# Performance work log

Measured on AMD Instinct MI355X. Metric: run time of the kernel, lower is better.

## Reference

```python
import jax, jax.numpy as jnp
import numpy as np
import math

BATCH, CLS, ATT_DIM, IMG_DIM = 256, 500, 1024, 1024
ATT_HC, HIDDEN_C = 256, 1024
T_TEMP = 10.0
DEGREE = 30
THRESH = math.cos(math.pi * DEGREE / 180.0)
NEG = -9.0e15


def setup_inputs() -> dict:
    key = jax.random.key(0)
    ks = jax.random.split(key, 9)
    inp = {
        "image_feats": jax.random.normal(ks[0], (BATCH, IMG_DIM), dtype=jnp.float32),
        "attributes": jax.random.normal(ks[1], (CLS, ATT_DIM), dtype=jnp.float32),
        "unused": 0,
        # learned parameters (kaiming-like scaling)
        "att_g": jax.random.normal(ks[2], (ATT_DIM, ATT_HC), dtype=jnp.float32) / math.sqrt(ATT_DIM),
        "img_w": jax.random.normal(ks[3], (IMG_DIM, HIDDEN_C), dtype=jnp.float32) / math.sqrt(IMG_DIM),
        "sem_w": jax.random.normal(ks[4], (ATT_DIM, HIDDEN_C), dtype=jnp.float32) / math.sqrt(ATT_DIM),
        "sem_b": jax.random.normal(ks[5], (1, HIDDEN_C), dtype=jnp.float32) / math.sqrt(IMG_DIM),
        "fc_w": jax.random.normal(ks[6], (1, HIDDEN_C), dtype=jnp.float32) / math.sqrt(HIDDEN_C),
        "fc_b": jax.random.normal(ks[7], (1,), dtype=jnp.float32) / math.sqrt(HIDDEN_C),
    }
    return inp


def _get_new_attribute(attributes, att_g):
    # project attributes, cosine similarity between all class pairs
    g = attributes @ att_g                                    # [cls, att_hC]
    gn = g / jnp.linalg.norm(g, axis=1, keepdims=True)        # row-normalize
    sim = gn @ gn.T                                           # [cls, cls] cosine sims
    raw = jnp.where(sim > THRESH, sim, NEG)                   # angular-threshold mask
    attention = jax.nn.softmax(raw * T_TEMP, axis=1)          # [cls, cls]
    return attention @ attributes                             # [cls, att_dim]


def reference(image_feats, attributes, unused, att_g, img_w, sem_w, sem_b, fc_w, fc_b):
    att_outs = _get_new_attribute(attributes, att_g)          # [cls, att_dim]
    # factor the broadcast: identical math to matmul on expanded tensors
    img_h = image_feats @ img_w                               # [batch, hidden]
    sem_h = att_outs @ sem_w                                  # [cls, hidden]
    hidden = jax.nn.relu(img_h[:, None, :] + sem_h[None, :, :] + sem_b[None, :, :])  # [batch, cls, hidden]
    out = jnp.einsum('bch,h->bc', hidden, fc_w[0]) + fc_b[0]  # [batch, cls]
    return out
```

## Files before the change

### kernel.cpp

```cpp
#include <hip/hip_runtime.h>
#include <math.h>

#define BATCH 256
#define CLS 500
#define T_TEMP_ 10.0f
#define THRESH_ 0.86602540378443864676f
#define NEGV -9.0e15f

typedef __attribute__((ext_vector_type(8))) short short8;
typedef __attribute__((ext_vector_type(8))) unsigned short u16x8;
typedef __attribute__((ext_vector_type(4))) unsigned short u16x4;
typedef __attribute__((ext_vector_type(4))) float f32x4;
typedef __attribute__((ext_vector_type(2))) float f32x2;

static __device__ __forceinline__ unsigned short f2bf(float x) {
    unsigned int u = __builtin_bit_cast(unsigned int, x);
    u += 0x7fff + ((u >> 16) & 1);
    return (unsigned short)(u >> 16);
}
static __device__ __forceinline__ float bf2f(unsigned short v) {
    return __builtin_bit_cast(float, (unsigned int)v << 16);
}
static __device__ __forceinline__ float fel(const float4& v, int j) { return (&v.x)[j]; }
static __device__ __forceinline__ u16x8 pack8(const float4& a, const float4& b) {
    u16x8 o;
    o[0] = f2bf(a.x); o[1] = f2bf(a.y); o[2] = f2bf(a.z); o[3] = f2bf(a.w);
    o[4] = f2bf(b.x); o[5] = f2bf(b.y); o[6] = f2bf(b.z); o[7] = f2bf(b.w);
    return o;
}

__global__ __launch_bounds__(256) void gpart_kernel(
    const float* __restrict__ attrs, const float* __restrict__ attg,
    float* __restrict__ gpart)
{
    __shared__ unsigned short As[64][40];
    __shared__ unsigned short Bs[128][40];
    const int t = threadIdx.x;
    const int bid = blockIdx.x;
    const int mt = bid >> 4, nt = (bid >> 3) & 1, split = bid & 7;
    const int n0 = nt * 128, ar0 = mt * 64, k0 = split * 128;

    const int w = t >> 6, lane = t & 63;
    const int wr = w >> 1, wc = w & 1;
    const int fr = lane & 15, kg = lane >> 4;
    const int as_row = t >> 2, as_kq = t & 3;
    const int bs_nc = (t & 31) * 4, bs_kr = t >> 5;

    f32x4 acc[2][4];
    #pragma unroll
    for (int i = 0; i < 2; ++i)
        #pragma unroll
        for (int j = 0; j < 4; ++j) acc[i][j] = (f32x4){0.f, 0.f, 0.f, 0.f};

    for (int kb = k0; kb < k0 + 128; kb += 32) {
        {
            const int gr = ar0 + as_row;
            float4 v0 = make_float4(0.f,0.f,0.f,0.f), v1 = v0;
            if (gr < CLS) {
                const float* ap = &attrs[(size_t)gr * 1024 + kb + as_kq * 8];
                v0 = *(const float4*)ap; v1 = *(const float4*)(ap + 4);
            }
            *(u16x8*)&As[as_row][as_kq * 8] = pack8(v0, v1);
        }
        {
            const float* bp = &attg[(size_t)(kb + bs_kr * 4) * 256 + n0 + bs_nc];
            float4 r0 = *(const float4*)(bp);
            float4 r1 = *(const float4*)(bp + 256);
            float4 r2 = *(const float4*)(bp + 512);
            float4 r3 = *(const float4*)(bp + 768);
            #pragma unroll
            for (int j = 0; j < 4; ++j) {
                unsigned int lo = (unsigned int)f2bf(fel(r0, j)) | ((unsigned int)f2bf(fel(r1, j)) << 16);
                unsigned int hi = (unsigned int)f2bf(fel(r2, j)) | ((unsigned int)f2bf(fel(r3, j)) << 16);
                uint2 u2; u2.x = lo; u2.y = hi;
                *(uint2*)&Bs[bs_nc + j][bs_kr * 4] = u2;
            }
        }
        __syncthreads();
        short8 af[2], bfr[4];
        #pragma unroll
        for (int i = 0; i < 2; ++i) af[i] = *(short8*)&As[wr * 32 + i * 16 + fr][kg * 8];
        #pragma unroll
        for (int j = 0; j < 4; ++j) bfr[j] = *(short8*)&Bs[wc * 64 + j * 16 + fr][kg * 8];
        #pragma unroll
        for (int i = 0; i < 2; ++i)
            #pragma unroll
            for (int j = 0; j < 4; ++j)
                acc[i][j] = __builtin_amdgcn_mfma_f32_16x16x32_bf16(af[i], bfr[j], acc[i][j], 0, 0, 0);
        __syncthreads();
    }

    float* Gp = gpart + (size_t)split * (512 * 256);
    const int orow0 = ar0 + wr * 32, ocol0 = n0 + wc * 64;
    #pragma unroll
    for (int i = 0; i < 2; ++i) {
        const int r0 = orow0 + i * 16 + kg * 4;
        #pragma unroll
        for (int j = 0; j < 4; ++j) {
            const int cc = ocol0 + j * 16 + fr;
            #pragma unroll
            for (int r = 0; r < 4; ++r)
                Gp[(size_t)(r0 + r) * 256 + cc] = acc[i][j][r];
        }
    }
}

__global__ __launch_bounds__(256) void reduce_norm_kernel(
    const float* __restrict__ part, unsigned short* __restrict__ gn_bf)
{
    const int c = blockIdx.x, t = threadIdx.x;
    float v = 0.f;
    #pragma unroll
    for (int z = 0; z < 8; ++z) v += part[(size_t)z * (512 * 256) + c * 256 + t];
    float ss = v * v;
    #pragma unroll
    for (int off = 32; off >= 1; off >>= 1) ss += __shfl_down(ss, off);
    __shared__ float red[4];
    const int wave = t >> 6, lane = t & 63;
    if (lane == 0) red[wave] = ss;
    __syncthreads();
    const float tot = red[0] + red[1] + red[2] + red[3];
    const float rn  = 1.f / sqrtf(tot);
    gn_bf[c * 256 + t] = f2bf(v * rn);
}

__global__ __launch_bounds__(256) void mfma_gemm_bf(
    const unsigned short* __restrict__ A1, int alim1,
    const unsigned short* __restrict__ A2, int a2t0, int alim2,
    const unsigned short* __restrict__ B1, const unsigned short* __restrict__ B2,
    float* __restrict__ C, unsigned short* __restrict__ Cbf,
    int M, int N, int K, int klen)
{
    __shared__ unsigned short As[64][40];
    __shared__ unsigned short Bs[128][40];

    const int t  = threadIdx.x;
    const int bx = blockIdx.x;
    const int n0 = blockIdx.y * 128;
    const int k0 = blockIdx.z * klen;

    const unsigned short* A; const unsigned short* B; int ar0, alim;
    if (bx < a2t0) { A = A1; B = B1; ar0 = bx * 64;          alim = alim1; }
    else           { A = A2; B = B2; ar0 = (bx - a2t0) * 64; alim = alim2; }

    const int w = t >> 6, lane = t & 63;
    const int wr = w >> 1, wc = w & 1;
    const int fr = lane & 15, kg = lane >> 4;

    const int a_row = t >> 2, a_k = (t & 3) * 8;
    const int b_row = t >> 1, b_k = (t & 1) * 16;
    const int gra = ar0 + a_row;
    const int grb = n0 + b_row;
    const bool va = gra < alim;
    const bool vb = grb < N;
    const size_t abase = (size_t)gra * K + a_k;
    const size_t bbase = (size_t)grb * K + b_k;

    u16x8 zz = {0,0,0,0,0,0,0,0};
    u16x8 pa = zz, pb0 = zz, pb1 = zz;
    if (va) pa = *(const u16x8*)&A[abase + k0];
    if (vb) { pb0 = *(const u16x8*)&B[bbase + k0]; pb1 = *(const u16x8*)&B[bbase + k0 + 8]; }

    f32x4 acc[2][4];
    #pragma unroll
    for (int i = 0; i < 2; ++i)
        #pragma unroll
        for (int j = 0; j < 4; ++j) acc[i][j] = (f32x4){0.f, 0.f, 0.f, 0.f};

    for (int kb = k0; kb < k0 + klen; kb += 32) {
        *(u16x8*)&As[a_row][a_k] = pa;
        *(u16x8*)&Bs[b_row][b_k] = pb0;
        *(u16x8*)&Bs[b_row][b_k + 8] = pb1;
        __syncthreads();

        const int kn = kb + 32;
        if (kn < k0 + klen) {
            if (va) pa = *(const u16x8*)&A[abase + kn];
            if (vb) { pb0 = *(const u16x8*)&B[bbase + kn]; pb1 = *(const u16x8*)&B[bbase + kn + 8]; }
        }

        short8 af[2], bfr[4];
        #pragma unroll
        for (int i = 0; i < 2; ++i) af[i] = *(short8*)&As[wr * 32 + i * 16 + fr][kg * 8];
        #pragma unroll
        for (int j = 0; j < 4; ++j) bfr[j] = *(short8*)&Bs[wc * 64 + j * 16 + fr][kg * 8];
        #pragma unroll
        for (int i = 0; i < 2; ++i)
            #pragma unroll
            for (int j = 0; j < 4; ++j)
                acc[i][j] = __builtin_amdgcn_mfma_f32_16x16x32_bf16(af[i], bfr[j], acc[i][j], 0, 0, 0);
        __syncthreads();
    }

    const int orow0 = bx * 64 + wr * 32, ocol0 = n0 + wc * 64;
    if (Cbf) {
        unsigned short* Cw = Cbf + (size_t)blockIdx.z * M * N;
        #pragma unroll
        for (int i = 0; i < 2; ++i) {
            const int r0 = orow0 + i * 16 + kg * 4;
            #pragma unroll
            for (int j = 0; j < 4; ++j) {
                const int cc = ocol0 + j * 16 + fr;
                if (cc >= N) continue;
                #pragma unroll
                for (int r = 0; r < 4; ++r) {
                    const int rr = r0 + r;
                    if (rr < M) Cw[(size_t)rr * N + cc] = f2bf(acc[i][j][r]);
                }
            }
        }
    } else {
        float* Cw = C + (gridDim.z > 1 ? (size_t)blockIdx.z * M * N : 0);
        #pragma unroll
        for (int i = 0; i < 2; ++i) {
            const int r0 = orow0 + i * 16 + kg * 4;
            #pragma unroll
            for (int j = 0; j < 4; ++j) {
                const int cc = ocol0 + j * 16 + fr;
                if (cc >= N) continue;
                #pragma unroll
                for (int r = 0; r < 4; ++r) {
                    const int rr = r0 + r;
                    if (rr < M) Cw[(size_t)rr * N + cc] = acc[i][j][r];
                }
            }
        }
    }
}

__global__ __launch_bounds__(256) void softmax_att_kernel(
    const float* __restrict__ sim, const float* __restrict__ attrs,
    unsigned short* __restrict__ att_outs)
{
    const int c = blockIdx.x, t = threadIdx.x;
    __shared__ float p_s[512];
    __shared__ float redm[4];
    __shared__ float reds[4];

    const float d0 = sim[(size_t)c * CLS + t];
    const float d1 = (t + 256 < CLS) ? sim[(size_t)c * CLS + t + 256] : NEGV;

    float vmax = fmaxf((d0 > THRESH_) ? d0 : NEGV, (d1 > THRESH_) ? d1 : NEGV);
    #pragma unroll
    for (int off = 32; off >= 1; off >>= 1) vmax = fmaxf(vmax, __shfl_down(vmax, off));
    const int wave = t >> 6, lane = t & 63;
    if (lane == 0) redm[wave] = vmax;
    __syncthreads();
    const float m = fmaxf(fmaxf(redm[0], redm[1]), fmaxf(redm[2], redm[3]));

    const float p0 = (d0 > THRESH_) ? expf(T_TEMP_ * (d0 - m)) : 0.f;
    const float p1 = (d1 > THRESH_) ? expf(T_TEMP_ * (d1 - m)) : 0.f;
    p_s[t] = p0;
    p_s[t + 256] = p1;
    float vsum = p0 + p1;
    #pragma unroll
    for (int off = 32; off >= 1; off >>= 1) vsum += __shfl_down(vsum, off);
    if (lane == 0) reds[wave] = vsum;
    __syncthreads();
    const float inv = 1.f / (reds[0] + reds[1] + reds[2] + reds[3]);

    float acc[4] = {0.f, 0.f, 0.f, 0.f};
    for (int base = 0; base < 512; base += 64) {
        const float pv_l = p_s[base + lane];
        unsigned long long mask = __ballot(pv_l > 0.f);
        while (mask) {
            const int l = __ffsll((long long)mask) - 1;
            mask &= mask - 1;
            const int c2 = base + l;
            const float pv = p_s[c2];
            const float* ar = &attrs[(size_t)c2 * 1024 + t];
            #pragma unroll
            for (int j = 0; j < 4; ++j) acc[j] += pv * ar[256 * j];
        }
    }
    #pragma unroll
    for (int j = 0; j < 4; ++j)
        att_outs[(size_t)c * 1024 + t + 256 * j] = f2bf(acc[j] * inv);
}

__global__ __launch_bounds__(256) void hid_kernel(
    const float* __restrict__ imgf, const unsigned short* __restrict__ atto_bf,
    const float* __restrict__ imgw, const float* __restrict__ semw,
    unsigned short* __restrict__ hidP)
{
    __shared__ unsigned short As[64][40];
    __shared__ unsigned short Bs[128][40];
    const int t = threadIdx.x;
    const int mt = blockIdx.x, nt = blockIdx.y, split = blockIdx.z;
    const int n0 = nt * 128, k0 = split * 256;
    const bool img_side = (mt < 4);
    const int ar0 = img_side ? mt * 64 : (mt - 4) * 64;
    const int alim = img_side ? 256 : 500;
    const float* Bf = img_side ? imgw : semw;

    const int w = t >> 6, lane = t & 63;
    const int wr = w >> 1, wc = w & 1;
    const int fr = lane & 15, kg = lane >> 4;
    const int as_row = t >> 2, as_kq = t & 3;
    const int bs_nc = (t & 31) * 4, bs_kr = t >> 5;

    f32x4 acc[2][4];
    #pragma unroll
    for (int i = 0; i < 2; ++i)
        #pragma unroll
        for (int j = 0; j < 4; ++j) acc[i][j] = (f32x4){0.f, 0.f, 0.f, 0.f};

    for (int kb = k0; kb < k0 + 256; kb += 32) {
        {
            const int gr = ar0 + as_row;
            if (img_side) {
                float4 v0 = make_float4(0.f,0.f,0.f,0.f), v1 = v0;
                if (gr < alim) {
                    const float* ap = &imgf[(size_t)gr * 1024 + kb + as_kq * 8];
                    v0 = *(const float4*)ap; v1 = *(const float4*)(ap + 4);
                }
                *(u16x8*)&As[as_row][as_kq * 8] = pack8(v0, v1);
            } else {
                u16x8 pa = {0,0,0,0,0,0,0,0};
                if (gr < alim) pa = *(const u16x8*)&atto_bf[(size_t)gr * 1024 + kb + as_kq * 8];
                *(u16x8*)&As[as_row][as_kq * 8] = pa;
            }
        }
        {
            const float* bp = &Bf[(size_t)(kb + bs_kr * 4) * 1024 + n0 + bs_nc];
            float4 r0 = *(const float4*)(bp);
            float4 r1 = *(const float4*)(bp + 1024);
            float4 r2 = *(const float4*)(bp + 2048);
            float4 r3 = *(const float4*)(bp + 3072);
            #pragma unroll
            for (int j = 0; j < 4; ++j) {
                unsigned int lo = (unsigned int)f2bf(fel(r0, j)) | ((unsigned int)f2bf(fel(r1, j)) << 16);
                unsigned int hi = (unsigned int)f2bf(fel(r2, j)) | ((unsigned int)f2bf(fel(r3, j)) << 16);
                uint2 u2; u2.x = lo; u2.y = hi;
                *(uint2*)&Bs[bs_nc + j][bs_kr * 4] = u2;
            }
        }
        __syncthreads();
        short8 af[2], bfr[4];
        #pragma unroll
        for (int i = 0; i < 2; ++i) af[i] = *(short8*)&As[wr * 32 + i * 16 + fr][kg * 8];
        #pragma unroll
        for (int j = 0; j < 4; ++j) bfr[j] = *(short8*)&Bs[wc * 64 + j * 16 + fr][kg * 8];
        #pragma unroll
        for (int i = 0; i < 2; ++i)
            #pragma unroll
            for (int j = 0; j < 4; ++j)
                acc[i][j] = __builtin_amdgcn_mfma_f32_16x16x32_bf16(af[i], bfr[j], acc[i][j], 0, 0, 0);
        __syncthreads();
    }

    unsigned short* Cw = hidP + (size_t)split * (756 * 1024);
    const int orow0 = mt * 64 + wr * 32, ocol0 = n0 + wc * 64;
    #pragma unroll
    for (int i = 0; i < 2; ++i) {
        const int r0 = orow0 + i * 16 + kg * 4;
        #pragma unroll
        for (int j = 0; j < 4; ++j) {
            const int cc = ocol0 + j * 16 + fr;
            #pragma unroll
            for (int r = 0; r < 4; ++r) {
                const int rr = r0 + r;
                if (rr < 756) Cw[(size_t)rr * 1024 + cc] = f2bf(acc[i][j][r]);
            }
        }
    }
}

__global__ __launch_bounds__(256) void fused_out_partial(
    const unsigned short* __restrict__ part, const float* __restrict__ sem_b,
    const float* __restrict__ fc_w, float* __restrict__ outpart)
{
    __shared__ float imgs[64][36];
    __shared__ float sems[64][36];
    __shared__ float fcs[32];

    const size_t pstride = (size_t)756 * 1024;
    const int t  = threadIdx.x;
    const int tb = t >> 4, tc = t & 15;
    const int b0 = blockIdx.x * 64, c0 = blockIdx.y * 64;
    const int h0 = blockIdx.z * 32;

    if (t < 8) *(float4*)&fcs[t * 4] = *(const float4*)&fc_w[h0 + t * 4];

    {
        const int row = t >> 2, col = (t & 3) * 8;
        f32x4 iv0 = {0.f,0.f,0.f,0.f}, iv1 = iv0;
        const unsigned short* pi = &part[(size_t)(b0 + row) * 1024 + h0 + col];
        #pragma unroll
        for (int z = 0; z < 4; ++z) {
            u16x8 vz = *(const u16x8*)(pi + (size_t)z * pstride);
            iv0[0] += bf2f(vz[0]); iv0[1] += bf2f(vz[1]);
            iv0[2] += bf2f(vz[2]); iv0[3] += bf2f(vz[3]);
            iv1[0] += bf2f(vz[4]); iv1[1] += bf2f(vz[5]);
            iv1[2] += bf2f(vz[6]); iv1[3] += bf2f(vz[7]);
        }
        *(f32x4*)&imgs[row][col]     = iv0;
        *(f32x4*)&imgs[row][col + 4] = iv1;

        f32x4 sv0 = {0.f,0.f,0.f,0.f}, sv1 = sv0;
        if (c0 + row < CLS) {
            const unsigned short* ps2 = &part[(size_t)(256 + c0 + row) * 1024 + h0 + col];
            #pragma unroll
            for (int z = 0; z < 4; ++z) {
                u16x8 vz = *(const u16x8*)(ps2 + (size_t)z * pstride);
                sv0[0] += bf2f(vz[0]); sv0[1] += bf2f(vz[1]);
                sv0[2] += bf2f(vz[2]); sv0[3] += bf2f(vz[3]);
                sv1[0] += bf2f(vz[4]); sv1[1] += bf2f(vz[5]);
                sv1[2] += bf2f(vz[6]); sv1[3] += bf2f(vz[7]);
            }
            sv0 += *(const f32x4*)&sem_b[h0 + col];
            sv1 += *(const f32x4*)&sem_b[h0 + col + 4];
        }
        *(f32x4*)&sems[row][col]     = sv0;
        *(f32x4*)&sems[row][col + 4] = sv1;
    }
    __syncthreads();

    f32x2 acc2[4][4];
    #pragma unroll
    for (int i = 0; i < 4; ++i)
        #pragma unroll
        for (int j = 0; j < 4; ++j) acc2[i][j] = (f32x2){0.f, 0.f};

    #pragma unroll
    for (int h4 = 0; h4 < 8; ++h4) {
        f32x4 ia[4], sa[4];
        #pragma unroll
        for (int i = 0; i < 4; ++i) ia[i] = *(f32x4*)&imgs[tb + 16 * i][h4 * 4];
        #pragma unroll
        for (int j = 0; j < 4; ++j) sa[j] = *(f32x4*)&sems[tc + 16 * j][h4 * 4];
        const f32x4 wv = *(const f32x4*)&fcs[h4 * 4];
        #pragma unroll
        for (int e2 = 0; e2 < 2; ++e2) {
            const f32x2 w2 = {wv[2 * e2], wv[2 * e2 + 1]};
            f32x2 ia2[4], sa2[4];
            #pragma unroll
            for (int i = 0; i < 4; ++i) ia2[i] = (f32x2){ia[i][2 * e2], ia[i][2 * e2 + 1]};
            #pragma unroll
            for (int j = 0; j < 4; ++j) sa2[j] = (f32x2){sa[j][2 * e2], sa[j][2 * e2 + 1]};
            #pragma unroll
            for (int i = 0; i < 4; ++i)
                #pragma unroll
                for (int j = 0; j < 4; ++j) {
                    f32x2 s = ia2[i] + sa2[j];
                    s = __builtin_elementwise_max(s, (f32x2){0.f, 0.f});
                    acc2[i][j] += s * w2;
                }
        }
    }

    const int nh = blockIdx.z;
    #pragma unroll
    for (int i = 0; i < 4; ++i) {
        const int b = b0 + tb + 16 * i;
        #pragma unroll
        for (int j = 0; j < 4; ++j) {
            const int cc = c0 + tc + 16 * j;
            if (cc < CLS)
                outpart[((size_t)nh * BATCH + b) * CLS + cc] = acc2[i][j][0] + acc2[i][j][1];
        }
    }
}

__global__ __launch_bounds__(256) void finalize_kernel(
    const float* __restrict__ partial, const float* __restrict__ fc_b,
    float* __restrict__ out)
{
    const int idx = blockIdx.x * 256 + threadIdx.x;
    if (idx >= BATCH * CLS) return;
    float s = fc_b[0];
    #pragma unroll
    for (int nh = 0; nh < 32; ++nh)
        s += partial[(size_t)nh * (BATCH * CLS) + idx];
    out[idx] = s;
}

extern "C" void kernel_launch(void* const* d_in, const int* in_sizes, int n_in,
                              void* d_out, int out_size, void* d_ws, size_t ws_size,
                              hipStream_t stream)
{
    const float* imgf  = (const float*)d_in[0];
    const float* attrs = (const float*)d_in[1];
    const float* attg  = (const float*)d_in[3];
    const float* imgw  = (const float*)d_in[4];
    const float* semw  = (const float*)d_in[5];
    const float* semb  = (const float*)d_in[6];
    const float* fcw   = (const float*)d_in[7];
    const float* fcb   = (const float*)d_in[8];
    float* out = (float*)d_out;

    char* ws = (char*)d_ws;
    size_t off = 0;
    auto alloc = [&](size_t b) { size_t o = off; off = (off + b + 255) & ~(size_t)255; return o; };
    float* gpart          = (float*)(ws + alloc((size_t)8 * 512 * 256 * 4));
    unsigned short* gn_bf = (unsigned short*)(ws + alloc((size_t)500 * 256 * 2));
    float* sim            = (float*)(ws + alloc((size_t)CLS * CLS * 4));
    unsigned short* atto  = (unsigned short*)(ws + alloc((size_t)500 * 1024 * 2));
    unsigned short* hidP  = (unsigned short*)(ws + alloc((size_t)4 * 756 * 1024 * 2));
    float* outP           = (float*)(ws + alloc((size_t)32 * BATCH * CLS * 4));

    gpart_kernel<<<128, 256, 0, stream>>>(attrs, attg, gpart);
    reduce_norm_kernel<<<CLS, 256, 0, stream>>>(gpart, gn_bf);
    mfma_gemm_bf<<<dim3(8, 4, 1), 256, 0, stream>>>(
        gn_bf, 500, gn_bf, 1000, 500, gn_bf, gn_bf,
        sim, nullptr, 500, 500, 256, 256);
    softmax_att_kernel<<<CLS, 256, 0, stream>>>(sim, attrs, atto);
    hid_kernel<<<dim3(12, 8, 4), 256, 0, stream>>>(imgf, atto, imgw, semw, hidP);
    fused_out_partial<<<dim3(4, 8, 32), 256, 0, stream>>>(hidP, semb, fcw, outP);
    finalize_kernel<<<(BATCH * CLS + 255) / 256, 256, 0, stream>>>(outP, fcb, out);
}
```

Baseline: 67.01 us.

## Reassociate attention matmul to gather projected attributes and fuse GEMMs into one launch

```diff
diff --git a/kernel.cpp b/kernel.cpp
--- a/kernel.cpp
+++ b/kernel.cpp
@@ -29,16 +29,17 @@
     return o;
 }
 
-__global__ __launch_bounds__(256) void gpart_kernel(
+__global__ __launch_bounds__(256) void mega_gemm(
     const float* __restrict__ attrs, const float* __restrict__ attg,
-    float* __restrict__ gpart)
+    const float* __restrict__ imgf, const float* __restrict__ imgw,
+    const float* __restrict__ semw,
+    float* __restrict__ gpart, unsigned short* __restrict__ imgP,
+    unsigned short* __restrict__ asemP)
 {
     __shared__ unsigned short As[64][40];
     __shared__ unsigned short Bs[128][40];
     const int t = threadIdx.x;
     const int bid = blockIdx.x;
-    const int mt = bid >> 4, nt = (bid >> 3) & 1, split = bid & 7;
-    const int n0 = nt * 128, ar0 = mt * 64, k0 = split * 128;
 
     const int w = t >> 6, lane = t & 63;
     const int wr = w >> 1, wc = w & 1;
@@ -46,28 +47,49 @@
     const int as_row = t >> 2, as_kq = t & 3;
     const int bs_nc = (t & 31) * 4, bs_kr = t >> 5;
 
+    const float* A; const float* Bf;
+    int ar0, alim, n0, k0, klen, bstride, split;
+    if (bid < 128) {
+        const int mt = bid >> 4, nt = (bid >> 3) & 1; split = bid & 7;
+        A = attrs; alim = CLS; ar0 = mt * 64;
+        Bf = attg; bstride = 256; n0 = nt * 128;
+        k0 = split * 128; klen = 128;
+    } else if (bid < 192) {
+        const int idx = bid - 128; split = idx & 1;
+        const int nt = (idx >> 1) & 7, mt = idx >> 4;
+        A = imgf; alim = 256; ar0 = mt * 64;
+        Bf = imgw; bstride = 1024; n0 = nt * 128;
+        k0 = split * 512; klen = 512;
+    } else {
+        const int idx = bid - 192; split = idx & 1;
+        const int nt = (idx >> 1) & 7, mt = idx >> 4;
+        A = attrs; alim = CLS; ar0 = mt * 64;
+        Bf = semw; bstride = 1024; n0 = nt * 128;
+        k0 = split * 512; klen = 512;
+    }
+
     f32x4 acc[2][4];
     #pragma unroll
     for (int i = 0; i < 2; ++i)
         #pragma unroll
         for (int j = 0; j < 4; ++j) acc[i][j] = (f32x4){0.f, 0.f, 0.f, 0.f};
 
-    for (int kb = k0; kb < k0 + 128; kb += 32) {
+    for (int kb = k0; kb < k0 + klen; kb += 32) {
         {
             const int gr = ar0 + as_row;
             float4 v0 = make_float4(0.f,0.f,0.f,0.f), v1 = v0;
-            if (gr < CLS) {
-                const float* ap = &attrs[(size_t)gr * 1024 + kb + as_kq * 8];
+            if (gr < alim) {
+                const float* ap = &A[(size_t)gr * 1024 + kb + as_kq * 8];
                 v0 = *(const float4*)ap; v1 = *(const float4*)(ap + 4);
             }
             *(u16x8*)&As[as_row][as_kq * 8] = pack8(v0, v1);
         }
         {
-            const float* bp = &attg[(size_t)(kb + bs_kr * 4) * 256 + n0 + bs_nc];
+            const float* bp = &Bf[(size_t)(kb + bs_kr * 4) * bstride + n0 + bs_nc];
             float4 r0 = *(const float4*)(bp);
-            float4 r1 = *(const float4*)(bp + 256);
-            float4 r2 = *(const float4*)(bp + 512);
-            float4 r3 = *(const float4*)(bp + 768);
+            float4 r1 = *(const float4*)(bp + bstride);
+            float4 r2 = *(const float4*)(bp + 2 * bstride);
+            float4 r3 = *(const float4*)(bp + 3 * bstride);
             #pragma unroll
             for (int j = 0; j < 4; ++j) {
                 unsigned int lo = (unsigned int)f2bf(fel(r0, j)) | ((unsigned int)f2bf(fel(r1, j)) << 16);
@@ -90,17 +112,34 @@
         __syncthreads();
     }
 
-    float* Gp = gpart + (size_t)split * (512 * 256);
     const int orow0 = ar0 + wr * 32, ocol0 = n0 + wc * 64;
-    #pragma unroll
-    for (int i = 0; i < 2; ++i) {
-        const int r0 = orow0 + i * 16 + kg * 4;
-        #pragma unroll
-        for (int j = 0; j < 4; ++j) {
-            const int cc = ocol0 + j * 16 + fr;
-            #pragma unroll
-            for (int r = 0; r < 4; ++r)
-                Gp[(size_t)(r0 + r) * 256 + cc] = acc[i][j][r];
+    if (bid < 128) {
+        float* Gp = gpart + (size_t)split * (512 * 256);
+        #pragma unroll
+        for (int i = 0; i < 2; ++i) {
+            const int r0 = orow0 + i * 16 + kg * 4;
+            #pragma unroll
+            for (int j = 0; j < 4; ++j) {
+                const int cc = ocol0 + j * 16 + fr;
+                #pragma unroll
+                for (int r = 0; r < 4; ++r)
+                    Gp[(size_t)(r0 + r) * 256 + cc] = acc[i][j][r];
+            }
+        }
+    } else {
+        unsigned short* Cw = (bid < 192)
+            ? imgP  + (size_t)split * (256 * 1024)
+            : asemP + (size_t)split * (512 * 1024);
+        #pragma unroll
+        for (int i = 0; i < 2; ++i) {
+            const int r0 = orow0 + i * 16 + kg * 4;
+            #pragma unroll
+            for (int j = 0; j < 4; ++j) {
+                const int cc = ocol0 + j * 16 + fr;
+                #pragma unroll
+                for (int r = 0; r < 4; ++r)
+                    Cw[(size_t)(r0 + r) * 1024 + cc] = f2bf(acc[i][j][r]);
+            }
         }
     }
 }
@@ -124,42 +163,31 @@
     gn_bf[c * 256 + t] = f2bf(v * rn);
 }
 
-__global__ __launch_bounds__(256) void mfma_gemm_bf(
-    const unsigned short* __restrict__ A1, int alim1,
-    const unsigned short* __restrict__ A2, int a2t0, int alim2,
-    const unsigned short* __restrict__ B1, const unsigned short* __restrict__ B2,
-    float* __restrict__ C, unsigned short* __restrict__ Cbf,
-    int M, int N, int K, int klen)
+__global__ __launch_bounds__(256) void sim_kernel(
+    const unsigned short* __restrict__ gn, float* __restrict__ S)
 {
     __shared__ unsigned short As[64][40];
     __shared__ unsigned short Bs[128][40];
-
     const int t  = threadIdx.x;
-    const int bx = blockIdx.x;
-    const int n0 = blockIdx.y * 128;
-    const int k0 = blockIdx.z * klen;
-
-    const unsigned short* A; const unsigned short* B; int ar0, alim;
-    if (bx < a2t0) { A = A1; B = B1; ar0 = bx * 64;          alim = alim1; }
-    else           { A = A2; B = B2; ar0 = (bx - a2t0) * 64; alim = alim2; }
+    const int ar0 = blockIdx.x * 64;
+    const int n0  = blockIdx.y * 128;
 
     const int w = t >> 6, lane = t & 63;
     const int wr = w >> 1, wc = w & 1;
     const int fr = lane & 15, kg = lane >> 4;
-
     const int a_row = t >> 2, a_k = (t & 3) * 8;
     const int b_row = t >> 1, b_k = (t & 1) * 16;
     const int gra = ar0 + a_row;
     const int grb = n0 + b_row;
-    const bool va = gra < alim;
-    const bool vb = grb < N;
-    const size_t abase = (size_t)gra * K + a_k;
-    const size_t bbase = (size_t)grb * K + b_k;
+    const bool va = gra < CLS;
+    const bool vb = grb < CLS;
+    const size_t abase = (size_t)gra * 256 + a_k;
+    const size_t bbase = (size_t)grb * 256 + b_k;
 
     u16x8 zz = {0,0,0,0,0,0,0,0};
     u16x8 pa = zz, pb0 = zz, pb1 = zz;
-    if (va) pa = *(const u16x8*)&A[abase + k0];
-    if (vb) { pb0 = *(const u16x8*)&B[bbase + k0]; pb1 = *(const u16x8*)&B[bbase + k0 + 8]; }
+    if (va) pa = *(const u16x8*)&gn[abase];
+    if (vb) { pb0 = *(const u16x8*)&gn[bbase]; pb1 = *(const u16x8*)&gn[bbase + 8]; }
 
     f32x4 acc[2][4];
     #pragma unroll
@@ -167,16 +195,16 @@
         #pragma unroll
         for (int j = 0; j < 4; ++j) acc[i][j] = (f32x4){0.f, 0.f, 0.f, 0.f};
 
-    for (int kb = k0; kb < k0 + klen; kb += 32) {
+    for (int kb = 0; kb < 256; kb += 32) {
         *(u16x8*)&As[a_row][a_k] = pa;
         *(u16x8*)&Bs[b_row][b_k] = pb0;
         *(u16x8*)&Bs[b_row][b_k + 8] = pb1;
         __syncthreads();
 
         const int kn = kb + 32;
-        if (kn < k0 + klen) {
-            if (va) pa = *(const u16x8*)&A[abase + kn];
-            if (vb) { pb0 = *(const u16x8*)&B[bbase + kn]; pb1 = *(const u16x8*)&B[bbase + kn + 8]; }
+        if (kn < 256) {
+            if (va) pa = *(const u16x8*)&gn[abase + kn];
+            if (vb) { pb0 = *(const u16x8*)&gn[bbase + kn]; pb1 = *(const u16x8*)&gn[bbase + kn + 8]; }
         }
 
         short8 af[2], bfr[4];
@@ -192,45 +220,26 @@
         __syncthreads();
     }
 
-    const int orow0 = bx * 64 + wr * 32, ocol0 = n0 + wc * 64;
-    if (Cbf) {
-        unsigned short* Cw = Cbf + (size_t)blockIdx.z * M * N;
-        #pragma unroll
-        for (int i = 0; i < 2; ++i) {
-            const int r0 = orow0 + i * 16 + kg * 4;
-            #pragma unroll
-            for (int j = 0; j < 4; ++j) {
-                const int cc = ocol0 + j * 16 + fr;
-                if (cc >= N) continue;
-                #pragma unroll
-                for (int r = 0; r < 4; ++r) {
-                    const int rr = r0 + r;
-                    if (rr < M) Cw[(size_t)rr * N + cc] = f2bf(acc[i][j][r]);
-                }
+    const int orow0 = ar0 + wr * 32, ocol0 = n0 + wc * 64;
+    #pragma unroll
+    for (int i = 0; i < 2; ++i) {
+        const int r0 = orow0 + i * 16 + kg * 4;
+        #pragma unroll
+        for (int j = 0; j < 4; ++j) {
+            const int cc = ocol0 + j * 16 + fr;
+            if (cc >= CLS) continue;
+            #pragma unroll
+            for (int r = 0; r < 4; ++r) {
+                const int rr = r0 + r;
+                if (rr < CLS) S[(size_t)rr * CLS + cc] = acc[i][j][r];
             }
         }
-    } else {
-        float* Cw = C + (gridDim.z > 1 ? (size_t)blockIdx.z * M * N : 0);
-        #pragma unroll
-        for (int i = 0; i < 2; ++i) {
-            const int r0 = orow0 + i * 16 + kg * 4;
-            #pragma unroll
-            for (int j = 0; j < 4; ++j) {
-                const int cc = ocol0 + j * 16 + fr;
-                if (cc >= N) continue;
-                #pragma unroll
-                for (int r = 0; r < 4; ++r) {
-                    const int rr = r0 + r;
-                    if (rr < M) Cw[(size_t)rr * N + cc] = acc[i][j][r];
-                }
-            }
-        }
-    }
-}
-
-__global__ __launch_bounds__(256) void softmax_att_kernel(
-    const float* __restrict__ sim, const float* __restrict__ attrs,
-    unsigned short* __restrict__ att_outs)
+    }
+}
+
+__global__ __launch_bounds__(256) void softmax_gather_kernel(
+    const float* __restrict__ sim, const unsigned short* __restrict__ asemP,
+    const float* __restrict__ semb, unsigned short* __restrict__ sem_h)
 {
     const int c = blockIdx.x, t = threadIdx.x;
     __shared__ float p_s[512];
@@ -268,113 +277,28 @@
             mask &= mask - 1;
             const int c2 = base + l;
             const float pv = p_s[c2];
-            const float* ar = &attrs[(size_t)c2 * 1024 + t];
-            #pragma unroll
-            for (int j = 0; j < 4; ++j) acc[j] += pv * ar[256 * j];
+            const unsigned short* a0 = &asemP[(size_t)c2 * 1024 + t];
+            const unsigned short* a1 = a0 + (size_t)512 * 1024;
+            #pragma unroll
+            for (int j = 0; j < 4; ++j)
+                acc[j] += pv * (bf2f(a0[256 * j]) + bf2f(a1[256 * j]));
         }
     }
     #pragma unroll
     for (int j = 0; j < 4; ++j)
-        att_outs[(size_t)c * 1024 + t + 256 * j] = f2bf(acc[j] * inv);
-}
-
-__global__ __launch_bounds__(256) void hid_kernel(
-    const float* __restrict__ imgf, const unsigned short* __restrict__ atto_bf,
-    const float* __restrict__ imgw, const float* __restrict__ semw,
-    unsigned short* __restrict__ hidP)
-{
-    __shared__ unsigned short As[64][40];
-    __shared__ unsigned short Bs[128][40];
-    const int t = threadIdx.x;
-    const int mt = blockIdx.x, nt = blockIdx.y, split = blockIdx.z;
-    const int n0 = nt * 128, k0 = split * 256;
-    const bool img_side = (mt < 4);
-    const int ar0 = img_side ? mt * 64 : (mt - 4) * 64;
-    const int alim = img_side ? 256 : 500;
-    const float* Bf = img_side ? imgw : semw;
-
-    const int w = t >> 6, lane = t & 63;
-    const int wr = w >> 1, wc = w & 1;
-    const int fr = lane & 15, kg = lane >> 4;
-    const int as_row = t >> 2, as_kq = t & 3;
-    const int bs_nc = (t & 31) * 4, bs_kr = t >> 5;
-
-    f32x4 acc[2][4];
-    #pragma unroll
-    for (int i = 0; i < 2; ++i)
-        #pragma unroll
-        for (int j = 0; j < 4; ++j) acc[i][j] = (f32x4){0.f, 0.f, 0.f, 0.f};
-
-    for (int kb = k0; kb < k0 + 256; kb += 32) {
-        {
-            const int gr = ar0 + as_row;
-            if (img_side) {
-                float4 v0 = make_float4(0.f,0.f,0.f,0.f), v1 = v0;
-                if (gr < alim) {
-                    const float* ap = &imgf[(size_t)gr * 1024 + kb + as_kq * 8];
-                    v0 = *(const float4*)ap; v1 = *(const float4*)(ap + 4);
-                }
-                *(u16x8*)&As[as_row][as_kq * 8] = pack8(v0, v1);
-            } else {
-                u16x8 pa = {0,0,0,0,0,0,0,0};
-                if (gr < alim) pa = *(const u16x8*)&atto_bf[(size_t)gr * 1024 + kb + as_kq * 8];
-                *(u16x8*)&As[as_row][as_kq * 8] = pa;
-            }
-        }
-        {
-            const float* bp = &Bf[(size_t)(kb + bs_kr * 4) * 1024 + n0 + bs_nc];
-            float4 r0 = *(const float4*)(bp);
-            float4 r1 = *(const float4*)(bp + 1024);
-            float4 r2 = *(const float4*)(bp + 2048);
-            float4 r3 = *(const float4*)(bp + 3072);
-            #pragma unroll
-            for (int j = 0; j < 4; ++j) {
-                unsigned int lo = (unsigned int)f2bf(fel(r0, j)) | ((unsigned int)f2bf(fel(r1, j)) << 16);
-                unsigned int hi = (unsigned int)f2bf(fel(r2, j)) | ((unsigned int)f2bf(fel(r3, j)) << 16);
-                uint2 u2; u2.x = lo; u2.y = hi;
-                *(uint2*)&Bs[bs_nc + j][bs_kr * 4] = u2;
-            }
-        }
-        __syncthreads();
-        short8 af[2], bfr[4];
-        #pragma unroll
-        for (int i = 0; i < 2; ++i) af[i] = *(short8*)&As[wr * 32 + i * 16 + fr][kg * 8];
-        #pragma unroll
-        for (int j = 0; j < 4; ++j) bfr[j] = *(short8*)&Bs[wc * 64 + j * 16 + fr][kg * 8];
-        #pragma unroll
-        for (int i = 0; i < 2; ++i)
-            #pragma unroll
-            for (int j = 0; j < 4; ++j)
-                acc[i][j] = __builtin_amdgcn_mfma_f32_16x16x32_bf16(af[i], bfr[j], acc[i][j], 0, 0, 0);
-        __syncthreads();
-    }
-
-    unsigned short* Cw = hidP + (size_t)split * (756 * 1024);
-    const int orow0 = mt * 64 + wr * 32, ocol0 = n0 + wc * 64;
-    #pragma unroll
-    for (int i = 0; i < 2; ++i) {
-        const int r0 = orow0 + i * 16 + kg * 4;
-        #pragma unroll
-        for (int j = 0; j < 4; ++j) {
-            const int cc = ocol0 + j * 16 + fr;
-            #pragma unroll
-            for (int r = 0; r < 4; ++r) {
-                const int rr = r0 + r;
-                if (rr < 756) Cw[(size_t)rr * 1024 + cc] = f2bf(acc[i][j][r]);
-            }
-        }
-    }
+        sem_h[(size_t)c * 1024 + t + 256 * j] =
+            f2bf(acc[j] * inv + semb[t + 256 * j]);
 }
 
 __global__ __launch_bounds__(256) void fused_out_partial(
-    const unsigned short* __restrict__ part, const float* __restrict__ sem_b,
+    const unsigned short* __restrict__ imgP, const unsigned short* __restrict__ sem_h,
     const float* __restrict__ fc_w, float* __restrict__ outpart)
 {
     __shared__ float imgs[64][36];
     __shared__ float sems[64][36];
     __shared__ float fcs[32];
 
-    const size_t pstride = (size_t)756 * 1024;
+    const size_t istride = (size_t)256 * 1024;
     const int t  = threadIdx.x;
     const int tb = t >> 4, tc = t & 15;
     const int b0 = blockIdx.x * 64, c0 = blockIdx.y * 64;
@@ -385,10 +309,10 @@
     {
         const int row = t >> 2, col = (t & 3) * 8;
         f32x4 iv0 = {0.f,0.f,0.f,0.f}, iv1 = iv0;
-        const unsigned short* pi = &part[(size_t)(b0 + row) * 1024 + h0 + col];
-        #pragma unroll
-        for (int z = 0; z < 4; ++z) {
-            u16x8 vz = *(const u16x8*)(pi + (size_t)z * pstride);
+        const unsigned short* pi = &imgP[(size_t)(b0 + row) * 1024 + h0 + col];
+        #pragma unroll
+        for (int z = 0; z < 2; ++z) {
+            u16x8 vz = *(const u16x8*)(pi + (size_t)z * istride);
             iv0[0] += bf2f(vz[0]); iv0[1] += bf2f(vz[1]);
             iv0[2] += bf2f(vz[2]); iv0[3] += bf2f(vz[3]);
             iv1[0] += bf2f(vz[4]); iv1[1] += bf2f(vz[5]);
@@ -399,17 +323,11 @@
 
         f32x4 sv0 = {0.f,0.f,0.f,0.f}, sv1 = sv0;
         if (c0 + row < CLS) {
-            const unsigned short* ps2 = &part[(size_t)(256 + c0 + row) * 1024 + h0 + col];
-            #pragma unroll
-            for (int z = 0; z < 4; ++z) {
-                u16x8 vz = *(const u16x8*)(ps2 + (size_t)z * pstride);
-                sv0[0] += bf2f(vz[0]); sv0[1] += bf2f(vz[1]);
-                sv0[2] += bf2f(vz[2]); sv0[3] += bf2f(vz[3]);
-                sv1[0] += bf2f(vz[4]); sv1[1] += bf2f(vz[5]);
-                sv1[2] += bf2f(vz[6]); sv1[3] += bf2f(vz[7]);
-            }
-            sv0 += *(const f32x4*)&sem_b[h0 + col];
-            sv1 += *(const f32x4*)&sem_b[h0 + col + 4];
+            u16x8 vz = *(const u16x8*)&sem_h[(size_t)(c0 + row) * 1024 + h0 + col];
+            sv0[0] = bf2f(vz[0]); sv0[1] = bf2f(vz[1]);
+            sv0[2] = bf2f(vz[2]); sv0[3] = bf2f(vz[3]);
+            sv1[0] = bf2f(vz[4]); sv1[1] = bf2f(vz[5]);
+            sv1[2] = bf2f(vz[6]); sv1[3] = bf2f(vz[7]);
         }
         *(f32x4*)&sems[row][col]     = sv0;
         *(f32x4*)&sems[row][col + 4] = sv1;
@@ -495,17 +413,16 @@
     float* gpart          = (float*)(ws + alloc((size_t)8 * 512 * 256 * 4));
     unsigned short* gn_bf = (unsigned short*)(ws + alloc((size_t)500 * 256 * 2));
     float* sim            = (float*)(ws + alloc((size_t)CLS * CLS * 4));
-    unsigned short* atto  = (unsigned short*)(ws + alloc((size_t)500 * 1024 * 2));
-    unsigned short* hidP  = (unsigned short*)(ws + alloc((size_t)4 * 756 * 1024 * 2));
+    unsigned short* imgP  = (unsigned short*)(ws + alloc((size_t)2 * 256 * 1024 * 2));
+    unsigned short* asemP = (unsigned short*)(ws + alloc((size_t)2 * 512 * 1024 * 2));
+    unsigned short* sem_h = (unsigned short*)(ws + alloc((size_t)500 * 1024 * 2));
     float* outP           = (float*)(ws + alloc((size_t)32 * BATCH * CLS * 4));
 
-    gpart_kernel<<<128, 256, 0, stream>>>(attrs, attg, gpart);
+    mega_gemm<<<320, 256, 0, stream>>>(attrs, attg, imgf, imgw, semw,
+                                       gpart, imgP, asemP);
     reduce_norm_kernel<<<CLS, 256, 0, stream>>>(gpart, gn_bf);
-    mfma_gemm_bf<<<dim3(8, 4, 1), 256, 0, stream>>>(
-        gn_bf, 500, gn_bf, 1000, 500, gn_bf, gn_bf,
-        sim, nullptr, 500, 500, 256, 256);
-    softmax_att_kernel<<<CLS, 256, 0, stream>>>(sim, attrs, atto);
-    hid_kernel<<<dim3(12, 8, 4), 256, 0, stream>>>(imgf, atto, imgw, semw, hidP);
-    fused_out_partial<<<dim3(4, 8, 32), 256, 0, stream>>>(hidP, semb, fcw, outP);
+    sim_kernel<<<dim3(8, 4), 256, 0, stream>>>(gn_bf, sim);
+    softmax_gather_kernel<<<CLS, 256, 0, stream>>>(sim, asemP, semb, sem_h);
+    fused_out_partial<<<dim3(4, 8, 32), 256, 0, stream>>>(imgP, sem_h, fcw, outP);
     finalize_kernel<<<(BATCH * CLS + 255) / 256, 256, 0, stream>>>(outP, fcb, out);
 }
```

New measurement: 64.44 us. 3.8% less time.
